# Kernel tuning notes

Hardware: AMD Instinct MI355X
Metric: run time of the kernel (lower is better)

Reference implementation:

```python
import jax, jax.numpy as jnp
import numpy as np

RES = 14
NUM_HEADS = 4
KEY_DIM = 16
ATTN_RATIO = 4
D = ATTN_RATIO * KEY_DIM          # 64, per-head value dim
DIM = NUM_HEADS * D               # 256, requires dim//heads == d for the cascade add
QKV_OUT = 2 * KEY_DIM + D         # 96
KSIZE = 5
BATCH = 512


def _make_bias_idxs(res=RES):
    # offset id for (|dr|,|dc|); ordering differs from torch's first-occurrence
    # order but is an equivalent relabeling of the 196 unique offsets.
    r = np.arange(res)
    row = np.repeat(r, res)
    col = np.tile(r, res)
    dr = np.abs(row[:, None] - row[None, :])
    dc = np.abs(col[:, None] - col[None, :])
    return jnp.asarray(dr * res + dc, dtype=jnp.int32)  # [N, N]


def setup_inputs() -> dict:
    key = jax.random.key(0)
    ks = jax.random.split(key, 12)
    c_head = DIM // NUM_HEADS
    return {
        "x": jax.random.normal(ks[0], (BATCH, DIM, RES, RES), jnp.float32),
        "qkv_w": jax.random.normal(ks[1], (NUM_HEADS, QKV_OUT, c_head), jnp.float32) * 0.1,
        "qkv_scale": jax.random.uniform(ks[2], (NUM_HEADS, QKV_OUT), jnp.float32, 0.5, 1.5),
        "qkv_bias": jax.random.normal(ks[3], (NUM_HEADS, QKV_OUT), jnp.float32) * 0.1,
        "dw_w": jax.random.normal(ks[4], (NUM_HEADS, KEY_DIM, KSIZE, KSIZE), jnp.float32) * 0.1,
        "dw_scale": jax.random.uniform(ks[5], (NUM_HEADS, KEY_DIM), jnp.float32, 0.5, 1.5),
        "dw_bias": jax.random.normal(ks[6], (NUM_HEADS, KEY_DIM), jnp.float32) * 0.1,
        "proj_w": jax.random.normal(ks[7], (DIM, NUM_HEADS * D), jnp.float32) * 0.05,
        "proj_scale": jax.random.uniform(ks[8], (DIM,), jnp.float32, 0.5, 1.5),
        "proj_bias": jax.random.normal(ks[9], (DIM,), jnp.float32) * 0.1,
        "attention_biases": jax.random.normal(ks[10], (NUM_HEADS, RES * RES), jnp.float32) * 0.02,
        "bias_idxs": _make_bias_idxs(),
    }


def reference(x, qkv_w, qkv_scale, qkv_bias, dw_w, dw_scale, dw_bias,
              proj_w, proj_scale, proj_bias, attention_biases, bias_idxs):
    B, C, H, W = x.shape
    h = qkv_w.shape[0]
    key_dim = dw_w.shape[1]
    d = qkv_w.shape[1] - 2 * key_dim
    scale = key_dim ** -0.5

    ab = attention_biases[:, bias_idxs]          # [h, N, N] relative-position bias
    feats_in = jnp.split(x, h, axis=1)           # h x [B, C/h, H, W]

    def affine(t, s, b):                          # eval-mode BN folded to per-channel affine
        return t * s[None, :, None, None] + b[None, :, None, None]

    outs = []
    feat = feats_in[0]
    for i in range(h):                            # structural cascade over heads
        if i > 0:
            feat = feat + feats_in[i]
        y = jnp.einsum('bchw,oc->bohw', feat, qkv_w[i])
        y = affine(y, qkv_scale[i], qkv_bias[i])
        q, k, v = y[:, :key_dim], y[:, key_dim:2 * key_dim], y[:, 2 * key_dim:]
        # depthwise conv + BN + GELU residual on q
        dq = jax.lax.conv_general_dilated(
            q, dw_w[i][:, None], (1, 1), 'SAME',
            dimension_numbers=('NCHW', 'OIHW', 'NCHW'),
            feature_group_count=key_dim)
        dq = affine(dq, dw_scale[i], dw_bias[i])
        q = jax.nn.gelu(dq, approximate=False) + q
        # attention over N = H*W tokens
        qf = q.reshape(B, key_dim, H * W)
        kf = k.reshape(B, key_dim, H * W)
        vf = v.reshape(B, d, H * W)
        attn = jnp.einsum('bcn,bcm->bnm', qf, kf) * scale + ab[i]
        attn = jax.nn.softmax(attn, axis=-1)
        feat = jnp.einsum('bdm,bnm->bdn', vf, attn).reshape(B, d, H, W)
        outs.append(feat)

    cat = jax.nn.relu(jnp.concatenate(outs, axis=1))
    out = jnp.einsum('bchw,oc->bohw', cat, proj_w)
    return affine(out, proj_scale, proj_bias)
```

## Files before the change

kernel.cpp:

```cpp
#include <hip/hip_runtime.h>
#include <math.h>

typedef _Float16 h2 __attribute__((ext_vector_type(2)));
typedef _Float16 f16x4 __attribute__((ext_vector_type(4)));
typedef float f32x4 __attribute__((ext_vector_type(4)));

#define NPOS 196
#define NH 4
#define KD 16
#define DV 64
#define DIM 256

#define MFMA16(A,B,C) __builtin_amdgcn_mfma_f32_16x16x16f16((A),(B),(C),0,0,0)

static __device__ __forceinline__ float fdot2(h2 a, h2 b, float c) {
#if __has_builtin(__builtin_amdgcn_fdot2)
    return __builtin_amdgcn_fdot2(a, b, c, false);
#else
    return fmaf((float)a.x, (float)b.x, fmaf((float)a.y, (float)b.y, c));
#endif
}
static __device__ __forceinline__ h2 pk(float a, float b) {
    h2 r; r.x = (_Float16)a; r.y = (_Float16)b; return r;
}
static __device__ __forceinline__ h2 pkz(float a, float b) {
#if __has_builtin(__builtin_amdgcn_cvt_pkrtz)
    return __builtin_bit_cast(h2, __builtin_amdgcn_cvt_pkrtz(a, b));
#else
    return pk(a, b);
#endif
}
union fhu { float f; h2 h; };
static __device__ __forceinline__ h2 as_h2(float f) { fhu u; u.f = f; return u.h; }
static __device__ __forceinline__ float as_f(h2 h) { fhu u; u.h = h; return u.f; }
static __device__ __forceinline__ f16x4 mk4(h2 a, h2 b) {
    union { f16x4 v; h2 h[2]; } u; u.h[0] = a; u.h[1] = b; return u.v;
}

__global__ void cga_prep(const float* __restrict__ pw, const float* __restrict__ qw,
                         h2* __restrict__ wh2, h2* __restrict__ qw2) {
    const int bid = blockIdx.x, t = threadIdx.x;
    if (bid < 128) {
        const int c2 = bid, o = t;
        wh2[c2 * DIM + o] = pk(pw[o * DIM + 2 * c2], pw[o * DIM + 2 * c2 + 1]);
    } else {
        const int idx = (bid - 128) * 256 + t;
        const int c2 = idx & 31, oo = idx >> 5;
        qw2[idx] = pk(qw[oo * 64 + 2 * c2], qw[oo * 64 + 2 * c2 + 1]);
    }
}

__global__ __launch_bounds__(256, 2) void cga_main(
    const float* __restrict__ x,
    const h2*    __restrict__ qw2,
    const float* __restrict__ qkv_s,
    const float* __restrict__ qkv_b,
    const float* __restrict__ dw_w,
    const float* __restrict__ dw_s,
    const float* __restrict__ dw_b,
    const float* __restrict__ ab,
    h2* __restrict__ catI)
{
    __shared__ __align__(16) char smem[65104];
    _Float16* xf = (_Float16*)smem;
    _Float16* vt = (_Float16*)(smem + 28288);
    float*    ql = (float*)(smem + 28288);
    _Float16* qn = (_Float16*)(smem + 55936);
    float*    bl = (float*)(smem + 64256);

    const int t  = threadIdx.x;
    const int l  = t & 63;
    const int w  = t >> 6;
    const int lr = l & 15;
    const int lq = l >> 4;
    const int b  = blockIdx.x;
    const bool act = t < NPOS;
    const int n  = act ? t : (NPOS - 1);
    const int rn = n / 14;
    const int cn = n - rn * 14;

    const float* xb = x + (size_t)b * (DIM * NPOS);

    if (act) {
#pragma unroll
        for (int c2 = 0; c2 < 32; ++c2)
            *(h2*)(xf + t * 68 + 2 * c2) =
                pk(xb[(2 * c2) * NPOS + t], xb[(2 * c2 + 1) * NPOS + t]);
    }
    if (t < 204) {
        int row = 196 + t / 17, off = t - (t / 17) * 17;
        *(float2*)(xf + row * 68 + off * 4) = make_float2(0.f, 0.f);
    }
    if (t < 60) {
        int row = 196 + t / 5, off = t - (t / 5) * 5;
        *(float2*)(qn + row * 20 + off * 4) = make_float2(0.f, 0.f);
    }
    __syncthreads();

    const f32x4 fz = {0.f, 0.f, 0.f, 0.f};

#pragma unroll 1
    for (int i = 0; i < NH; ++i) {
        const _Float16* wq = (const _Float16*)qw2 + (size_t)i * (96 * 64);
        const float* sc = qkv_s + i * 96;
        const float* bi = qkv_b + i * 96;

        if (t < NPOS)      bl[t] = ab[i * NPOS + t] - 4.0f;
        else if (t < 212)  bl[t] = 0.f;

        {
            f16x4 aq0 = *(const f16x4*)(wq + lr * 64 +  0 + lq * 4);
            f16x4 aq1 = *(const f16x4*)(wq + lr * 64 + 16 + lq * 4);
            f16x4 aq2 = *(const f16x4*)(wq + lr * 64 + 32 + lq * 4);
            f16x4 aq3 = *(const f16x4*)(wq + lr * 64 + 48 + lq * 4);
            float s0 = sc[lq * 4 + 0], s1 = sc[lq * 4 + 1];
            float s2 = sc[lq * 4 + 2], s3 = sc[lq * 4 + 3];
            float b0 = bi[lq * 4 + 0], b1 = bi[lq * 4 + 1];
            float b2 = bi[lq * 4 + 2], b3 = bi[lq * 4 + 3];
#pragma unroll 1
            for (int nt = w; nt < 13; nt += 4) {
                const _Float16* xr = xf + (nt * 16 + lr) * 68;
                f32x4 acc = fz;
                acc = MFMA16(aq0, *(const f16x4*)(xr +  0 + lq * 4), acc);
                acc = MFMA16(aq1, *(const f16x4*)(xr + 16 + lq * 4), acc);
                acc = MFMA16(aq2, *(const f16x4*)(xr + 32 + lq * 4), acc);
                acc = MFMA16(aq3, *(const f16x4*)(xr + 48 + lq * 4), acc);
                int nn = nt * 16 + lr;
                if (nn < NPOS) {
                    ql[(lq * 4 + 0) * NPOS + nn] = fmaf(acc[0], s0, b0);
                    ql[(lq * 4 + 1) * NPOS + nn] = fmaf(acc[1], s1, b1);
                    ql[(lq * 4 + 2) * NPOS + nn] = fmaf(acc[2], s2, b2);
                    ql[(lq * 4 + 3) * NPOS + nn] = fmaf(acc[3], s3, b3);
                }
            }
        }
        __syncthreads();

        {
            const float* dww = dw_w + i * (KD * 25);
            const float* dws = dw_s + i * KD;
            const float* dwb = dw_b + i * KD;
            float q2[KD];
#pragma unroll
            for (int ch = 0; ch < KD; ++ch) {
                float s = 0.f;
#pragma unroll
                for (int kr = 0; kr < 5; ++kr) {
                    int rr = rn + kr - 2;
                    bool rok = (unsigned)rr < 14u;
#pragma unroll
                    for (int kc = 0; kc < 5; ++kc) {
                        int cc = cn + kc - 2;
                        bool ok = rok && ((unsigned)cc < 14u);
                        int idx = ok ? (rr * 14 + cc) : n;
                        float qv = ql[ch * NPOS + idx];
                        qv = ok ? qv : 0.f;
                        s = fmaf(qv, dww[ch * 25 + kr * 5 + kc], s);
                    }
                }
                float dv = fmaf(s, dws[ch], dwb[ch]);
                float g = 0.5f * dv * (1.f + erff(dv * 0.70710678118654752f));
                q2[ch] = g + ql[ch * NPOS + n];
            }
            if (act) {
#pragma unroll
                for (int e = 0; e < 8; ++e)
                    *(h2*)(qn + n * 20 + 2 * e) = pk(q2[2 * e], q2[2 * e + 1]);
            }
        }
        __syncthreads();

        f16x4 kf[13];
        {
            f16x4 ak0 = *(const f16x4*)(wq + (16 + lr) * 64 +  0 + lq * 4);
            f16x4 ak1 = *(const f16x4*)(wq + (16 + lr) * 64 + 16 + lq * 4);
            f16x4 ak2 = *(const f16x4*)(wq + (16 + lr) * 64 + 32 + lq * 4);
            f16x4 ak3 = *(const f16x4*)(wq + (16 + lr) * 64 + 48 + lq * 4);
            float ks0 = sc[16 + lq * 4 + 0], ks1 = sc[16 + lq * 4 + 1];
            float ks2 = sc[16 + lq * 4 + 2], ks3 = sc[16 + lq * 4 + 3];
            float kb0 = bi[16 + lq * 4 + 0], kb1 = bi[16 + lq * 4 + 1];
            float kb2 = bi[16 + lq * 4 + 2], kb3 = bi[16 + lq * 4 + 3];
#pragma unroll
            for (int mt = 0; mt < 13; ++mt) {
                const _Float16* xr = xf + (mt * 16 + lr) * 68;
                f32x4 acc = fz;
                acc = MFMA16(ak0, *(const f16x4*)(xr +  0 + lq * 4), acc);
                acc = MFMA16(ak1, *(const f16x4*)(xr + 16 + lq * 4), acc);
                acc = MFMA16(ak2, *(const f16x4*)(xr + 32 + lq * 4), acc);
                acc = MFMA16(ak3, *(const f16x4*)(xr + 48 + lq * 4), acc);
                kf[mt] = mk4(pk(fmaf(acc[0], ks0, kb0), fmaf(acc[1], ks1, kb1)),
                             pk(fmaf(acc[2], ks2, kb2), fmaf(acc[3], ks3, kb3)));
            }
            f16x4 av[16];
            float vs[16], vb[16];
#pragma unroll
            for (int ot = 0; ot < 4; ++ot) {
#pragma unroll
                for (int k4 = 0; k4 < 4; ++k4)
                    av[ot * 4 + k4] = *(const f16x4*)(wq + (32 + ot * 16 + lr) * 64
                                                      + k4 * 16 + lq * 4);
#pragma unroll
                for (int j = 0; j < 4; ++j) {
                    vs[ot * 4 + j] = sc[32 + ot * 16 + lq * 4 + j];
                    vb[ot * 4 + j] = bi[32 + ot * 16 + lq * 4 + j];
                }
            }
#pragma unroll 1
            for (int nt = w; nt < 13; nt += 4) {
                const _Float16* xr = xf + (nt * 16 + lr) * 68;
                f16x4 bx0 = *(const f16x4*)(xr +  0 + lq * 4);
                f16x4 bx1 = *(const f16x4*)(xr + 16 + lq * 4);
                f16x4 bx2 = *(const f16x4*)(xr + 32 + lq * 4);
                f16x4 bx3 = *(const f16x4*)(xr + 48 + lq * 4);
                int m = nt * 16 + lr;
                bool mok = m < NPOS;
#pragma unroll
                for (int ot = 0; ot < 4; ++ot) {
                    f32x4 acc = fz;
                    acc = MFMA16(av[ot * 4 + 0], bx0, acc);
                    acc = MFMA16(av[ot * 4 + 1], bx1, acc);
                    acc = MFMA16(av[ot * 4 + 2], bx2, acc);
                    acc = MFMA16(av[ot * 4 + 3], bx3, acc);
                    if (mok) {
#pragma unroll
                        for (int j = 0; j < 4; ++j)
                            vt[(ot * 16 + lq * 4 + j) * 216 + m] =
                                (_Float16)fmaf(acc[j], vs[ot * 4 + j], vb[ot * 4 + j]);
                    }
                }
            }
            if (t < 192) {
                int row = t / 3, off = t - (t / 3) * 3;
                *(float2*)(vt + row * 216 + 196 + off * 4) = make_float2(0.f, 0.f);
            }
        }
        __syncthreads();

        h2* cb = catI + ((size_t)b * 128 + i * 32) * NPOS;
        const float* xnp = xb + (size_t)(i + 1) * (DV * NPOS);
        const bool more = (i < NH - 1);
#pragma unroll 1
        for (int nt = w; nt < 13; nt += 4) {
            int nn = nt * 16 + lr;
            bool nok = nn < NPOS;
            int rnn = (nn * 4682) >> 16;
            int cnn = nn - rnn * 14;
            f16x4 qb = *(const f16x4*)(qn + nn * 20 + lq * 4);
            f16x4 pf[13];
            float den = 0.f;
#pragma unroll
            for (int mt = 0; mt < 13; ++mt) {
                f32x4 sv = MFMA16(kf[mt], qb, fz);
                float p0, p1, p2, p3;
                {
                    int m0 = mt * 16 + lq * 4;
                    int rm0 = (m0 * 4682) >> 16;       int cm0 = m0 - rm0 * 14;
                    int rm1 = ((m0 + 1) * 4682) >> 16; int cm1 = m0 + 1 - rm1 * 14;
                    int rm2 = ((m0 + 2) * 4682) >> 16; int cm2 = m0 + 2 - rm2 * 14;
                    int rm3 = ((m0 + 3) * 4682) >> 16; int cm3 = m0 + 3 - rm3 * 14;
                    int dr0 = rnn - rm0; dr0 = dr0 < 0 ? -dr0 : dr0;
                    int dr1 = rnn - rm1; dr1 = dr1 < 0 ? -dr1 : dr1;
                    int dr2 = rnn - rm2; dr2 = dr2 < 0 ? -dr2 : dr2;
                    int dr3 = rnn - rm3; dr3 = dr3 < 0 ? -dr3 : dr3;
                    int dc0 = cnn - cm0; dc0 = dc0 < 0 ? -dc0 : dc0;
                    int dc1 = cnn - cm1; dc1 = dc1 < 0 ? -dc1 : dc1;
                    int dc2 = cnn - cm2; dc2 = dc2 < 0 ? -dc2 : dc2;
                    int dc3 = cnn - cm3; dc3 = dc3 < 0 ? -dc3 : dc3;
                    p0 = __expf(fmaf(sv[0], 0.25f, bl[dr0 * 14 + dc0]));
                    p1 = __expf(fmaf(sv[1], 0.25f, bl[dr1 * 14 + dc1]));
                    p2 = __expf(fmaf(sv[2], 0.25f, bl[dr2 * 14 + dc2]));
                    p3 = __expf(fmaf(sv[3], 0.25f, bl[dr3 * 14 + dc3]));
                    if (m0 + 3 >= NPOS) {
                        p0 = (m0 + 0 < NPOS) ? p0 : 0.f;
                        p1 = (m0 + 1 < NPOS) ? p1 : 0.f;
                        p2 = (m0 + 2 < NPOS) ? p2 : 0.f;
                        p3 = (m0 + 3 < NPOS) ? p3 : 0.f;
                    }
                }
                den += p0 + p1 + p2 + p3;
                pf[mt] = mk4(pkz(p0, p1), pkz(p2, p3));
            }
            den += __shfl_xor(den, 16, 64);
            den += __shfl_xor(den, 32, 64);
            float inv = 1.f / den;

            f32x4 o0 = fz, o1 = fz, o2 = fz, o3 = fz;
#pragma unroll
            for (int mt = 0; mt < 13; ++mt) {
                const _Float16* vr = vt + mt * 16 + lq * 4;
                o0 = MFMA16(*(const f16x4*)(vr + ( 0 + lr) * 216), pf[mt], o0);
                o1 = MFMA16(*(const f16x4*)(vr + (16 + lr) * 216), pf[mt], o1);
                o2 = MFMA16(*(const f16x4*)(vr + (32 + lr) * 216), pf[mt], o2);
                o3 = MFMA16(*(const f16x4*)(vr + (48 + lr) * 216), pf[mt], o3);
            }
            if (nok) {
                auto epi = [&](f32x4 oa, int dt) {
                    float v0 = oa[0] * inv, v1 = oa[1] * inv;
                    float v2 = oa[2] * inv, v3 = oa[3] * inv;
                    int c2 = dt * 8 + lq * 2;
                    cb[c2 * NPOS + nn]       = pk(fmaxf(v0, 0.f), fmaxf(v1, 0.f));
                    cb[(c2 + 1) * NPOS + nn] = pk(fmaxf(v2, 0.f), fmaxf(v3, 0.f));
                    if (more) {
                        int c0 = dt * 16 + lq * 4;
                        f16x4 fw = mk4(pk(v0 + xnp[(c0 + 0) * NPOS + nn],
                                          v1 + xnp[(c0 + 1) * NPOS + nn]),
                                       pk(v2 + xnp[(c0 + 2) * NPOS + nn],
                                          v3 + xnp[(c0 + 3) * NPOS + nn]));
                        *(f16x4*)(xf + nn * 68 + c0) = fw;
                    }
                };
                epi(o0, 0); epi(o1, 1); epi(o2, 2); epi(o3, 3);
            }
        }
        __syncthreads();
    }
}

__global__ __launch_bounds__(256, 4) void cga_proj(
    const h2* __restrict__ catI, const h2* __restrict__ wh2,
    const float* __restrict__ ps, const float* __restrict__ pb,
    float* __restrict__ out)
{
    __shared__ __align__(16) h2 cl[128 * 28];
    const int t = threadIdx.x;
    const int b = blockIdx.x / 7;
    const int nc = blockIdx.x - b * 7;
    const int n0 = nc * 28;

    const h2* cb = catI + (size_t)b * (128 * NPOS) + n0;
    for (int idx = t; idx < 128 * 7; idx += 256) {
        int c2 = idx / 7;
        int j4 = idx - c2 * 7;
        *(float4*)&cl[c2 * 28 + j4 * 4] = *(const float4*)&cb[c2 * NPOS + j4 * 4];
    }
    __syncthreads();

    float acc[28];
#pragma unroll
    for (int j = 0; j < 28; ++j) acc[j] = 0.f;

    const h2* wcol = wh2 + t;
    h2 wv[8];
#pragma unroll
    for (int j = 0; j < 8; ++j) wv[j] = wcol[j * DIM];

#pragma unroll 1
    for (int c8 = 0; c8 < 16; ++c8) {
        h2 wn[8];
#pragma unroll
        for (int j = 0; j < 8; ++j)
            wn[j] = wcol[(((c8 * 8) + 8 + j) & 127) * DIM];
#pragma unroll
        for (int j = 0; j < 8; ++j) {
            h2 w = wv[j];
            const float4* cf = (const float4*)&cl[(c8 * 8 + j) * 28];
#pragma unroll
            for (int j4 = 0; j4 < 7; ++j4) {
                float4 cv = cf[j4];
                acc[j4 * 4 + 0] = fdot2(w, as_h2(cv.x), acc[j4 * 4 + 0]);
                acc[j4 * 4 + 1] = fdot2(w, as_h2(cv.y), acc[j4 * 4 + 1]);
                acc[j4 * 4 + 2] = fdot2(w, as_h2(cv.z), acc[j4 * 4 + 2]);
                acc[j4 * 4 + 3] = fdot2(w, as_h2(cv.w), acc[j4 * 4 + 3]);
            }
        }
#pragma unroll
        for (int j = 0; j < 8; ++j) wv[j] = wn[j];
    }

    float s = ps[t], bb = pb[t];
    float* ob = out + ((size_t)b * DIM + t) * NPOS + n0;
#pragma unroll
    for (int j = 0; j < 28; ++j) ob[j] = fmaf(acc[j], s, bb);
}

extern "C" void kernel_launch(void* const* d_in, const int* in_sizes, int n_in,
                              void* d_out, int out_size, void* d_ws, size_t ws_size,
                              hipStream_t stream) {
    const float* x      = (const float*)d_in[0];
    const float* qkv_w  = (const float*)d_in[1];
    const float* qkv_s  = (const float*)d_in[2];
    const float* qkv_b  = (const float*)d_in[3];
    const float* dw_w   = (const float*)d_in[4];
    const float* dw_s   = (const float*)d_in[5];
    const float* dw_b   = (const float*)d_in[6];
    const float* proj_w = (const float*)d_in[7];
    const float* proj_s = (const float*)d_in[8];
    const float* proj_b = (const float*)d_in[9];
    const float* ab     = (const float*)d_in[10];
    float* out = (float*)d_out;

    h2* wh2  = (h2*)d_ws;
    h2* qw2  = (h2*)((char*)d_ws + 131072);
    h2* catI = (h2*)((char*)d_ws + 180224);

    cga_prep<<<176, 256, 0, stream>>>(proj_w, qkv_w, wh2, qw2);
    cga_main<<<512, 256, 0, stream>>>(x, qw2, qkv_s, qkv_b,
                                      dw_w, dw_s, dw_b, ab, catI);
    cga_proj<<<512 * 7, 256, 0, stream>>>(catI, wh2, proj_s, proj_b, out);
}
```

Measured before the change: 509.8 us.

## Use MFMA for output projection with fragment-layout intermediate and 512-thread blocks

Replaces the fdot2-based projection kernel with an MFMA 16x16x16 kernel that reads the concatenated head outputs directly in MFMA B-fragment layout. The main kernel now writes those pre-swizzled fragments and runs with 512 threads, splitting the depthwise conv channels and the tile loops across twice as many waves. The projection weights are pre-swizzled into A-fragment layout in the prep kernel. The aim is to remove the scalar dot-product cost of the projection and its shared-memory staging, and to raise parallelism in the main kernel. In exchange there are more register-resident weight fragments per wave and possible occupancy pressure from the larger blocks.

```diff
diff --git a/kernel.cpp b/kernel.cpp
--- a/kernel.cpp
+++ b/kernel.cpp
@@ -13,13 +13,6 @@
 
 #define MFMA16(A,B,C) __builtin_amdgcn_mfma_f32_16x16x16f16((A),(B),(C),0,0,0)
 
-static __device__ __forceinline__ float fdot2(h2 a, h2 b, float c) {
-#if __has_builtin(__builtin_amdgcn_fdot2)
-    return __builtin_amdgcn_fdot2(a, b, c, false);
-#else
-    return fmaf((float)a.x, (float)b.x, fmaf((float)a.y, (float)b.y, c));
-#endif
-}
 static __device__ __forceinline__ h2 pk(float a, float b) {
     h2 r; r.x = (_Float16)a; r.y = (_Float16)b; return r;
 }
@@ -30,27 +23,32 @@
     return pk(a, b);
 #endif
 }
-union fhu { float f; h2 h; };
-static __device__ __forceinline__ h2 as_h2(float f) { fhu u; u.f = f; return u.h; }
-static __device__ __forceinline__ float as_f(h2 h) { fhu u; u.h = h; return u.f; }
 static __device__ __forceinline__ f16x4 mk4(h2 a, h2 b) {
     union { f16x4 v; h2 h[2]; } u; u.h[0] = a; u.h[1] = b; return u.v;
 }
 
 __global__ void cga_prep(const float* __restrict__ pw, const float* __restrict__ qw,
-                         h2* __restrict__ wh2, h2* __restrict__ qw2) {
+                         _Float16* __restrict__ pwh, h2* __restrict__ qw2) {
     const int bid = blockIdx.x, t = threadIdx.x;
-    if (bid < 128) {
-        const int c2 = bid, o = t;
-        wh2[c2 * DIM + o] = pk(pw[o * DIM + 2 * c2], pw[o * DIM + 2 * c2 + 1]);
+    if (bid < 64) {
+        const int e = bid * 256 + t;
+        const int l = e & 63;
+        const int kt = (e >> 6) & 15;
+        const int ot = e >> 10;
+        const int lr = l & 15, lq = l >> 4;
+        f16x4 v;
+#pragma unroll
+        for (int j = 0; j < 4; ++j)
+            v[j] = (_Float16)pw[(ot * 16 + lr) * DIM + kt * 16 + lq * 4 + j];
+        *(f16x4*)(pwh + (size_t)e * 4) = v;
     } else {
-        const int idx = (bid - 128) * 256 + t;
+        const int idx = (bid - 64) * 256 + t;
         const int c2 = idx & 31, oo = idx >> 5;
         qw2[idx] = pk(qw[oo * 64 + 2 * c2], qw[oo * 64 + 2 * c2 + 1]);
     }
 }
 
-__global__ __launch_bounds__(256, 2) void cga_main(
+__global__ __launch_bounds__(512, 2) void cga_main(
     const float* __restrict__ x,
     const h2*    __restrict__ qw2,
     const float* __restrict__ qkv_s,
@@ -59,7 +57,7 @@
     const float* __restrict__ dw_s,
     const float* __restrict__ dw_b,
     const float* __restrict__ ab,
-    h2* __restrict__ catI)
+    _Float16* __restrict__ frag)
 {
     __shared__ __align__(16) char smem[65104];
     _Float16* xf = (_Float16*)smem;
@@ -75,17 +73,26 @@
     const int lq = l >> 4;
     const int b  = blockIdx.x;
     const bool act = t < NPOS;
-    const int n  = act ? t : (NPOS - 1);
-    const int rn = n / 14;
-    const int cn = n - rn * 14;
+    const int cg  = t >> 8;
+    const int tc  = t & 255;
+    const bool cact = tc < NPOS;
+    const int np  = cact ? tc : (NPOS - 1);
+    const int rn  = np / 14;
+    const int cn  = np - rn * 14;
 
     const float* xb = x + (size_t)b * (DIM * NPOS);
 
     if (act) {
 #pragma unroll
-        for (int c2 = 0; c2 < 32; ++c2)
+        for (int c2 = 0; c2 < 16; ++c2)
             *(h2*)(xf + t * 68 + 2 * c2) =
                 pk(xb[(2 * c2) * NPOS + t], xb[(2 * c2 + 1) * NPOS + t]);
+    }
+    if (cg == 1 && cact) {
+#pragma unroll
+        for (int c2 = 16; c2 < 32; ++c2)
+            *(h2*)(xf + np * 68 + 2 * c2) =
+                pk(xb[(2 * c2) * NPOS + np], xb[(2 * c2 + 1) * NPOS + np]);
     }
     if (t < 204) {
         int row = 196 + t / 17, off = t - (t / 17) * 17;
@@ -118,7 +125,7 @@
             float b0 = bi[lq * 4 + 0], b1 = bi[lq * 4 + 1];
             float b2 = bi[lq * 4 + 2], b3 = bi[lq * 4 + 3];
 #pragma unroll 1
-            for (int nt = w; nt < 13; nt += 4) {
+            for (int nt = w; nt < 13; nt += 8) {
                 const _Float16* xr = xf + (nt * 16 + lr) * 68;
                 f32x4 acc = fz;
                 acc = MFMA16(aq0, *(const f16x4*)(xr +  0 + lq * 4), acc);
@@ -137,12 +144,14 @@
         __syncthreads();
 
         {
+            const int ch0 = 8 * cg;
             const float* dww = dw_w + i * (KD * 25);
             const float* dws = dw_s + i * KD;
             const float* dwb = dw_b + i * KD;
-            float q2[KD];
-#pragma unroll
-            for (int ch = 0; ch < KD; ++ch) {
+            float q2[8];
+#pragma unroll
+            for (int ch = 0; ch < 8; ++ch) {
+                const int c = ch0 + ch;
                 float s = 0.f;
 #pragma unroll
                 for (int kr = 0; kr < 5; ++kr) {
@@ -152,20 +161,20 @@
                     for (int kc = 0; kc < 5; ++kc) {
                         int cc = cn + kc - 2;
                         bool ok = rok && ((unsigned)cc < 14u);
-                        int idx = ok ? (rr * 14 + cc) : n;
-                        float qv = ql[ch * NPOS + idx];
+                        int idx = ok ? (rr * 14 + cc) : np;
+                        float qv = ql[c * NPOS + idx];
                         qv = ok ? qv : 0.f;
-                        s = fmaf(qv, dww[ch * 25 + kr * 5 + kc], s);
+                        s = fmaf(qv, dww[c * 25 + kr * 5 + kc], s);
                     }
                 }
-                float dv = fmaf(s, dws[ch], dwb[ch]);
+                float dv = fmaf(s, dws[c], dwb[c]);
                 float g = 0.5f * dv * (1.f + erff(dv * 0.70710678118654752f));
-                q2[ch] = g + ql[ch * NPOS + n];
-            }
-            if (act) {
-#pragma unroll
-                for (int e = 0; e < 8; ++e)
-                    *(h2*)(qn + n * 20 + 2 * e) = pk(q2[2 * e], q2[2 * e + 1]);
+                q2[ch] = g + ql[c * NPOS + np];
+            }
+            if (cact) {
+#pragma unroll
+                for (int e = 0; e < 4; ++e)
+                    *(h2*)(qn + np * 20 + ch0 + 2 * e) = pk(q2[2 * e], q2[2 * e + 1]);
             }
         }
         __syncthreads();
@@ -206,7 +215,7 @@
                 }
             }
 #pragma unroll 1
-            for (int nt = w; nt < 13; nt += 4) {
+            for (int nt = w; nt < 13; nt += 8) {
                 const _Float16* xr = xf + (nt * 16 + lr) * 68;
                 f16x4 bx0 = *(const f16x4*)(xr +  0 + lq * 4);
                 f16x4 bx1 = *(const f16x4*)(xr + 16 + lq * 4);
@@ -236,11 +245,11 @@
         }
         __syncthreads();
 
-        h2* cb = catI + ((size_t)b * 128 + i * 32) * NPOS;
+        _Float16* fh = frag + ((size_t)b * 16 + i * 4) * (13 * 256);
         const float* xnp = xb + (size_t)(i + 1) * (DV * NPOS);
         const bool more = (i < NH - 1);
 #pragma unroll 1
-        for (int nt = w; nt < 13; nt += 4) {
+        for (int nt = w; nt < 13; nt += 8) {
             int nn = nt * 16 + lr;
             bool nok = nn < NPOS;
             int rnn = (nn * 4682) >> 16;
@@ -293,13 +302,13 @@
                 o2 = MFMA16(*(const f16x4*)(vr + (32 + lr) * 216), pf[mt], o2);
                 o3 = MFMA16(*(const f16x4*)(vr + (48 + lr) * 216), pf[mt], o3);
             }
-            if (nok) {
-                auto epi = [&](f32x4 oa, int dt) {
+            auto epi = [&](f32x4 oa, int dt) {
+                f16x4 st;
+                if (nok) {
                     float v0 = oa[0] * inv, v1 = oa[1] * inv;
                     float v2 = oa[2] * inv, v3 = oa[3] * inv;
-                    int c2 = dt * 8 + lq * 2;
-                    cb[c2 * NPOS + nn]       = pk(fmaxf(v0, 0.f), fmaxf(v1, 0.f));
-                    cb[(c2 + 1) * NPOS + nn] = pk(fmaxf(v2, 0.f), fmaxf(v3, 0.f));
+                    st = mk4(pk(fmaxf(v0, 0.f), fmaxf(v1, 0.f)),
+                             pk(fmaxf(v2, 0.f), fmaxf(v3, 0.f)));
                     if (more) {
                         int c0 = dt * 16 + lq * 4;
                         f16x4 fw = mk4(pk(v0 + xnp[(c0 + 0) * NPOS + nn],
@@ -308,69 +317,66 @@
                                           v3 + xnp[(c0 + 3) * NPOS + nn]));
                         *(f16x4*)(xf + nn * 68 + c0) = fw;
                     }
-                };
-                epi(o0, 0); epi(o1, 1); epi(o2, 2); epi(o3, 3);
-            }
+                } else {
+                    st[0] = st[1] = st[2] = st[3] = (_Float16)0.f;
+                }
+                *(f16x4*)(fh + (dt * 13 + nt) * 256 + l * 4) = st;
+            };
+            epi(o0, 0); epi(o1, 1); epi(o2, 2); epi(o3, 3);
         }
         __syncthreads();
     }
 }
 
-__global__ __launch_bounds__(256, 4) void cga_proj(
-    const h2* __restrict__ catI, const h2* __restrict__ wh2,
+__global__ __launch_bounds__(512, 2) void cga_proj(
+    const _Float16* __restrict__ frag,
+    const _Float16* __restrict__ pwh,
     const float* __restrict__ ps, const float* __restrict__ pb,
     float* __restrict__ out)
 {
-    __shared__ __align__(16) h2 cl[128 * 28];
     const int t = threadIdx.x;
-    const int b = blockIdx.x / 7;
-    const int nc = blockIdx.x - b * 7;
-    const int n0 = nc * 28;
-
-    const h2* cb = catI + (size_t)b * (128 * NPOS) + n0;
-    for (int idx = t; idx < 128 * 7; idx += 256) {
-        int c2 = idx / 7;
-        int j4 = idx - c2 * 7;
-        *(float4*)&cl[c2 * 28 + j4 * 4] = *(const float4*)&cb[c2 * NPOS + j4 * 4];
-    }
-    __syncthreads();
-
-    float acc[28];
-#pragma unroll
-    for (int j = 0; j < 28; ++j) acc[j] = 0.f;
-
-    const h2* wcol = wh2 + t;
-    h2 wv[8];
-#pragma unroll
-    for (int j = 0; j < 8; ++j) wv[j] = wcol[j * DIM];
-
+    const int l = t & 63;
+    const int w = t >> 6;
+    const int lr = l & 15, lq = l >> 4;
+    const int b = blockIdx.x;
+    const int ot0 = 2 * w;
+
+    f16x4 a0[16], a1[16];
+#pragma unroll
+    for (int kt = 0; kt < 16; ++kt) {
+        a0[kt] = *(const f16x4*)(pwh + (size_t)((ot0 * 16 + kt) * 64 + l) * 4);
+        a1[kt] = *(const f16x4*)(pwh + (size_t)(((ot0 + 1) * 16 + kt) * 64 + l) * 4);
+    }
+    float s0[4], bb0[4], s1[4], bb1[4];
+#pragma unroll
+    for (int j = 0; j < 4; ++j) {
+        s0[j]  = ps[ot0 * 16 + lq * 4 + j];
+        bb0[j] = pb[ot0 * 16 + lq * 4 + j];
+        s1[j]  = ps[(ot0 + 1) * 16 + lq * 4 + j];
+        bb1[j] = pb[(ot0 + 1) * 16 + lq * 4 + j];
+    }
+
+    const _Float16* fb = frag + (size_t)b * (16 * 13 * 256);
+    const f32x4 fz = {0.f, 0.f, 0.f, 0.f};
 #pragma unroll 1
-    for (int c8 = 0; c8 < 16; ++c8) {
-        h2 wn[8];
-#pragma unroll
-        for (int j = 0; j < 8; ++j)
-            wn[j] = wcol[(((c8 * 8) + 8 + j) & 127) * DIM];
-#pragma unroll
-        for (int j = 0; j < 8; ++j) {
-            h2 w = wv[j];
-            const float4* cf = (const float4*)&cl[(c8 * 8 + j) * 28];
-#pragma unroll
-            for (int j4 = 0; j4 < 7; ++j4) {
-                float4 cv = cf[j4];
-                acc[j4 * 4 + 0] = fdot2(w, as_h2(cv.x), acc[j4 * 4 + 0]);
-                acc[j4 * 4 + 1] = fdot2(w, as_h2(cv.y), acc[j4 * 4 + 1]);
-                acc[j4 * 4 + 2] = fdot2(w, as_h2(cv.z), acc[j4 * 4 + 2]);
-                acc[j4 * 4 + 3] = fdot2(w, as_h2(cv.w), acc[j4 * 4 + 3]);
-            }
-        }
-#pragma unroll
-        for (int j = 0; j < 8; ++j) wv[j] = wn[j];
-    }
-
-    float s = ps[t], bb = pb[t];
-    float* ob = out + ((size_t)b * DIM + t) * NPOS + n0;
-#pragma unroll
-    for (int j = 0; j < 28; ++j) ob[j] = fmaf(acc[j], s, bb);
+    for (int nt = 0; nt < 13; ++nt) {
+        f32x4 acc0 = fz, acc1 = fz;
+#pragma unroll
+        for (int kt = 0; kt < 16; ++kt) {
+            f16x4 bf = *(const f16x4*)(fb + (kt * 13 + nt) * 256 + l * 4);
+            acc0 = MFMA16(a0[kt], bf, acc0);
+            acc1 = MFMA16(a1[kt], bf, acc1);
+        }
+        int nn = nt * 16 + lr;
+        if (nn < NPOS) {
+            float* ob = out + (size_t)b * (DIM * NPOS) + nn;
+#pragma unroll
+            for (int j = 0; j < 4; ++j) {
+                ob[(ot0 * 16 + lq * 4 + j) * NPOS] = fmaf(acc0[j], s0[j], bb0[j]);
+                ob[((ot0 + 1) * 16 + lq * 4 + j) * NPOS] = fmaf(acc1[j], s1[j], bb1[j]);
+            }
+        }
+    }
 }
 
 extern "C" void kernel_launch(void* const* d_in, const int* in_sizes, int n_in,
@@ -389,12 +395,12 @@
     const float* ab     = (const float*)d_in[10];
     float* out = (float*)d_out;
 
-    h2* wh2  = (h2*)d_ws;
-    h2* qw2  = (h2*)((char*)d_ws + 131072);
-    h2* catI = (h2*)((char*)d_ws + 180224);
-
-    cga_prep<<<176, 256, 0, stream>>>(proj_w, qkv_w, wh2, qw2);
-    cga_main<<<512, 256, 0, stream>>>(x, qw2, qkv_s, qkv_b,
-                                      dw_w, dw_s, dw_b, ab, catI);
-    cga_proj<<<512 * 7, 256, 0, stream>>>(catI, wh2, proj_s, proj_b, out);
-}
+    _Float16* pwh  = (_Float16*)d_ws;
+    h2*       qw2  = (h2*)((char*)d_ws + 131072);
+    _Float16* frag = (_Float16*)((char*)d_ws + 180224);
+
+    cga_prep<<<112, 256, 0, stream>>>(proj_w, qkv_w, pwh, qw2);
+    cga_main<<<512, 512, 0, stream>>>(x, qw2, qkv_s, qkv_b,
+                                      dw_w, dw_s, dw_b, ab, frag);
+    cga_proj<<<512, 512, 0, stream>>>(frag, pwh, proj_s, proj_b, out);
+}
```

Result: slower. 968.5 us (+90.0%).
